# Kernel optimization log

Measured on AMD Instinct MI355X. Metric: run time of the kernel, lower is better.

Reference implementation:

```python
import jax, jax.numpy as jnp
import numpy as np

L, B, S, D, H, DK, F = 6, 4, 2048, 512, 8, 64, 2048


def setup_inputs() -> dict:
    key = jax.random.key(0)
    ks = iter(jax.random.split(key, 40))
    def rn(shape, scale=0.02):
        return jax.random.normal(next(ks), shape, jnp.float32) * scale
    inp = {
        "x": jax.random.normal(next(ks), (B, S, D), jnp.float32),
        "enc": jax.random.normal(next(ks), (B, S, D), jnp.float32),
    }
    for pre in ("sa", "ca"):
        inp[f"{pre}_wq"] = rn((L, D, H * DK)); inp[f"{pre}_bq"] = jnp.zeros((L, H * DK), jnp.float32)
        inp[f"{pre}_wk"] = rn((L, D, H * DK)); inp[f"{pre}_bk"] = jnp.zeros((L, H * DK), jnp.float32)
        inp[f"{pre}_wv"] = rn((L, D, H * DK)); inp[f"{pre}_bv"] = jnp.zeros((L, H * DK), jnp.float32)
        inp[f"{pre}_wo"] = rn((L, H * DK, D)); inp[f"{pre}_bo"] = jnp.zeros((L, D), jnp.float32)
    for i in (1, 2, 3):
        inp[f"ln{i}_g"] = jnp.ones((L, D), jnp.float32)
        inp[f"ln{i}_b"] = jnp.zeros((L, D), jnp.float32)
    inp["ff_w1"] = rn((L, D, F)); inp["ff_b1"] = jnp.zeros((L, F), jnp.float32)
    inp["ff_w2"] = rn((L, F, D)); inp["ff_b2"] = jnp.zeros((L, D), jnp.float32)
    return inp


def _layer_norm(z, g, b, eps=1e-5):
    m = z.mean(-1, keepdims=True)
    v = z.var(-1, keepdims=True)
    return (z - m) * jax.lax.rsqrt(v + eps) * g + b


def _mha(q_in, kv_in, wq, bq, wk, bk, wv, bv, wo, bo, causal_bias):
    b, s, _ = q_in.shape
    Q = (q_in @ wq + bq).reshape(b, s, H, DK)   # [B,S,H,DK]
    K = (kv_in @ wk + bk).reshape(b, s, H, DK)
    V = (kv_in @ wv + bv).reshape(b, s, H, DK)
    scores = jnp.einsum("bqhd,bkhd->bhqk", Q, K) / jnp.float32(DK) ** 0.5
    if causal_bias is not None:
        scores = scores + causal_bias  # additive -inf above diagonal
    w = jax.nn.softmax(scores, axis=-1)
    att = jnp.einsum("bhqk,bkhd->bqhd", w, V).reshape(b, s, H * DK)
    return att @ wo + bo


def reference(x, enc, sa_wq, sa_bq, sa_wk, sa_bk, sa_wv, sa_bv, sa_wo, sa_bo,
              ca_wq, ca_bq, ca_wk, ca_bk, ca_wv, ca_bv, ca_wo, ca_bo,
              ln1_g, ln1_b, ln2_g, ln2_b, ln3_g, ln3_b,
              ff_w1, ff_b1, ff_w2, ff_b2):
    s = x.shape[1]
    causal_bias = jnp.triu(jnp.full((s, s), -jnp.inf, jnp.float32), 1)

    params = (sa_wq, sa_bq, sa_wk, sa_bk, sa_wv, sa_bv, sa_wo, sa_bo,
              ca_wq, ca_bq, ca_wk, ca_bk, ca_wv, ca_bv, ca_wo, ca_bo,
              ln1_g, ln1_b, ln2_g, ln2_b, ln3_g, ln3_b,
              ff_w1, ff_b1, ff_w2, ff_b2)

    def block(h, p):
        (swq, sbq, swk, sbk, swv, sbv, swo, sbo,
         cwq, cbq, cwk, cbk, cwv, cbv, cwo, cbo,
         g1, b1, g2, b2, g3, b3, w1, bb1, w2, bb2) = p
        # masked self-attention + residual + LN  (faithful to source)
        x1 = _layer_norm(h + _mha(h, h, swq, sbq, swk, sbk, swv, sbv, swo, sbo, causal_bias), g1, b1)
        # cross-attention; residual comes from the BLOCK INPUT h (source bug kept)
        y = _layer_norm(h + _mha(x1, enc, cwq, cbq, cwk, cbk, cwv, cbv, cwo, cbo, None), g2, b2)
        # FFN; residual from x1 (source bug kept)
        out = _layer_norm(x1 + (jax.nn.relu(y @ w1 + bb1) @ w2 + bb2), g3, b3)
        return out, None

    out, _ = jax.lax.scan(block, x, params)
    return out
```

## Files before the change

kernel.cpp:

```cpp
#include <hip/hip_runtime.h>
#include <stdint.h>

#define LCOUNT 6
#define BB 4
#define SS 2048
#define DD 512
#define HH 8
#define DKK 64
#define FFDIM 2048
#define MM (BB*SS)

typedef __attribute__((ext_vector_type(8))) __bf16 bf16x8;
typedef __attribute__((ext_vector_type(4))) float f32x4;
typedef unsigned short u16;

__device__ __forceinline__ u16 f2bf(float f) {
  union { __bf16 h; u16 u; } v; v.h = (__bf16)f; return v.u;
}
__device__ __forceinline__ float bf2f(u16 u) {
  union { uint32_t u; float f; } v; v.u = ((uint32_t)u) << 16;
  return v.f;
}

__device__ __forceinline__ void gload_lds16(const u16* gsrc, u16* ldst) {
  __builtin_amdgcn_global_load_lds((const __attribute__((address_space(1))) char*)gsrc,
                                   (__attribute__((address_space(3))) char*)ldst, 16, 0, 0);
}

__global__ __launch_bounds__(256) void f2bf_kernel(const float* __restrict__ in,
                                                   u16* __restrict__ outp, int n) {
  int i = (blockIdx.x * 256 + threadIdx.x) * 8;
  if (i >= n) return;
  float4 a = *(const float4*)&in[i];
  float4 b = *(const float4*)&in[i + 4];
  union { u16 us[8]; uint4 v; } pk;
  pk.us[0] = f2bf(a.x); pk.us[1] = f2bf(a.y); pk.us[2] = f2bf(a.z); pk.us[3] = f2bf(a.w);
  pk.us[4] = f2bf(b.x); pk.us[5] = f2bf(b.y); pk.us[6] = f2bf(b.z); pk.us[7] = f2bf(b.w);
  *(uint4*)&outp[i] = pk.v;
}

__global__ __launch_bounds__(256) void bias_cat(const float* a, const float* b, const float* c,
                                                float* dst, int n, int total) {
  int i = blockIdx.x * 256 + threadIdx.x;
  if (i >= total) return;
  int parts = (c != nullptr) ? 3 : 2;
  int per = parts * n;
  int l = i / per, cc = i % per;
  const float* s = cc < n ? a : (cc < 2 * n ? b : c);
  dst[i] = s[l * n + (cc % n)];
}

__global__ __launch_bounds__(256) void wtrans(const float* __restrict__ W,
                                              u16* __restrict__ Wt, int K_, int N_,
                                              size_t lstride) {
  __shared__ float tile[64 * 65];
  const int l = blockIdx.z;
  const float* Wl = W + (size_t)l * K_ * N_;
  u16* Wtl = Wt + (size_t)l * lstride;
  const int n0 = blockIdx.x * 64, k0 = blockIdx.y * 64;
  const int tid = threadIdx.x;
  const int r = tid >> 2, c4 = (tid & 3) * 16;
#pragma unroll
  for (int j = 0; j < 16; j += 4) {
    float4 v = *(const float4*)&Wl[(size_t)(k0 + r) * N_ + n0 + c4 + j];
    tile[r * 65 + c4 + j + 0] = v.x;
    tile[r * 65 + c4 + j + 1] = v.y;
    tile[r * 65 + c4 + j + 2] = v.z;
    tile[r * 65 + c4 + j + 3] = v.w;
  }
  __syncthreads();
  const int nr = tid >> 2, kc = (tid & 3) * 16;
#pragma unroll
  for (int half = 0; half < 2; ++half) {
    union { u16 us[8]; uint4 v; } pk;
#pragma unroll
    for (int e = 0; e < 8; ++e) pk.us[e] = f2bf(tile[(kc + half * 8 + e) * 65 + nr]);
    *(uint4*)&Wtl[(size_t)(n0 + nr) * K_ + k0 + kc + half * 8] = pk.v;
  }
}

struct WtBatch {
  const float* src[8];
  u16* dst[8];
  unsigned long long lstr[8];
};
__global__ __launch_bounds__(256) void wtrans8(WtBatch wb) {
  __shared__ float tile[64 * 65];
  const int z = blockIdx.z;
  const int slot = z / 6, l = z - slot * 6;
  const float* Wl = wb.src[slot] + (size_t)l * 512 * 512;
  u16* Wtl = wb.dst[slot] + (size_t)l * wb.lstr[slot];
  const int n0 = blockIdx.x * 64, k0 = blockIdx.y * 64;
  const int tid = threadIdx.x;
  const int r = tid >> 2, c4 = (tid & 3) * 16;
#pragma unroll
  for (int j = 0; j < 16; j += 4) {
    float4 v = *(const float4*)&Wl[(size_t)(k0 + r) * 512 + n0 + c4 + j];
    tile[r * 65 + c4 + j + 0] = v.x;
    tile[r * 65 + c4 + j + 1] = v.y;
    tile[r * 65 + c4 + j + 2] = v.z;
    tile[r * 65 + c4 + j + 3] = v.w;
  }
  __syncthreads();
  const int nr = tid >> 2, kc = (tid & 3) * 16;
#pragma unroll
  for (int half = 0; half < 2; ++half) {
    union { u16 us[8]; uint4 v; } pk;
#pragma unroll
    for (int e = 0; e < 8; ++e) pk.us[e] = f2bf(tile[(kc + half * 8 + e) * 65 + nr]);
    *(uint4*)&Wtl[(size_t)(n0 + nr) * 512 + k0 + kc + half * 8] = pk.v;
  }
}

template <int BMT, int BNT, int BKT, bool RELU, bool VT>
__global__ __launch_bounds__(256)
void gemm_bt(const u16* __restrict__ A, const u16* __restrict__ Bt,
             const float* __restrict__ bias, u16* __restrict__ C,
             int N_, int K_, int CS, u16* __restrict__ vt, int vtc0,
             const u16* __restrict__ A2, int a2col) {
  constexpr int MR = BMT / 32;
  constexpr int NR = BNT / 32;
  constexpr int CH = BKT / 8;
  constexpr int RPR = 2048 / BKT;
  constexpr int KS = BKT / 32;
  __shared__ u16 As[BMT * BKT];
  __shared__ u16 Bs[BNT * BKT];
  const int tid = threadIdx.x;
  const int wid = tid >> 6, lane = tid & 63;
  const int l15 = lane & 15, g = lane >> 4;
  const int wr = wid >> 1, wc = wid & 1;
  const int lrow = (CH == 8) ? (lane >> 3) : (lane >> 4);
  const int lch  = lane & (CH - 1);
  const int wrows = 64 / CH;
  const int lin = blockIdx.x + gridDim.x * blockIdx.y;
  const int nwg = gridDim.x * gridDim.y;
  const int swz = (lin & 7) * (nwg >> 3) + (lin >> 3);
  const int brow = (swz / gridDim.x) * BMT;
  const int bcol = (swz % gridDim.x) * BNT;
  const u16* Ap = (A2 != nullptr && bcol >= a2col) ? A2 : A;

  f32x4 acc[MR][NR];
#pragma unroll
  for (int m = 0; m < MR; ++m)
#pragma unroll
    for (int n = 0; n < NR; ++n) acc[m][n] = (f32x4){0.f, 0.f, 0.f, 0.f};

  for (int kt = 0; kt < K_; kt += BKT) {
#pragma unroll
    for (int r = 0; r < BMT / RPR; ++r) {
      int row = r * RPR + wid * wrows + lrow;
      int slot = lch ^ (row & 7);
      gload_lds16(Ap + (size_t)(brow + row) * K_ + kt + slot * 8,
                  &As[r * 2048 + wid * 512]);
    }
#pragma unroll
    for (int r = 0; r < BNT / RPR; ++r) {
      int row = r * RPR + wid * wrows + lrow;
      int slot = lch ^ (row & 7);
      gload_lds16(Bt + (size_t)(bcol + row) * K_ + kt + slot * 8,
                  &Bs[r * 2048 + wid * 512]);
    }
    __syncthreads();
#pragma unroll
    for (int ks = 0; ks < KS; ++ks) {
      bf16x8 af[MR], bfr[NR];
#pragma unroll
      for (int m = 0; m < MR; ++m) {
        int row = wr * (BMT / 2) + m * 16 + l15;
        int slot = (ks * 4 + g) ^ (row & 7);
        af[m] = *(const bf16x8*)&As[row * BKT + slot * 8];
      }
#pragma unroll
      for (int n = 0; n < NR; ++n) {
        int row = wc * (BNT / 2) + n * 16 + l15;
        int slot = (ks * 4 + g) ^ (row & 7);
        bfr[n] = *(const bf16x8*)&Bs[row * BKT + slot * 8];
      }
#pragma unroll
      for (int m = 0; m < MR; ++m)
#pragma unroll
        for (int n = 0; n < NR; ++n)
          acc[m][n] = __builtin_amdgcn_mfma_f32_16x16x32_bf16(af[m], bfr[n], acc[m][n], 0, 0, 0);
    }
    __syncthreads();
  }
#pragma unroll
  for (int n = 0; n < NR; ++n) {
    int col = bcol + wc * (BNT / 2) + n * 16 + l15;
    float bv = bias ? bias[col] : 0.f;
    if (VT && col >= vtc0) {
      int hh = (col - vtc0) >> 6, dd = (col - vtc0) & 63;
#pragma unroll
      for (int m = 0; m < MR; ++m) {
        int s0g = brow + wr * (BMT / 2) + m * 16 + g * 4;
        int bb = s0g >> 11, ss = s0g & (SS - 1);
        union { u16 us[4]; uint2 v; } pk;
#pragma unroll
        for (int r = 0; r < 4; ++r) pk.us[r] = f2bf(acc[m][n][r] + bv);
        *(uint2*)&vt[(((size_t)(bb * HH + hh)) * DKK + dd) * SS + ss] = pk.v;
      }
    } else {
#pragma unroll
      for (int m = 0; m < MR; ++m) {
#pragma unroll
        for (int r = 0; r < 4; ++r) {
          int rowg = brow + wr * (BMT / 2) + m * 16 + g * 4 + r;
          float v = acc[m][n][r] + bv;
          if (RELU) v = fmaxf(v, 0.f);
          C[(size_t)rowg * CS + col] = f2bf(v);
        }
      }
    }
  }
}

__global__ __launch_bounds__(256)
void gemm_ln(const u16* __restrict__ A, const u16* __restrict__ Bt,
             const float* __restrict__ bias, const u16* __restrict__ Res,
             const float* __restrict__ gamma, const float* __restrict__ beta,
             u16* __restrict__ Out, float* __restrict__ Ofp, int K_) {
  __shared__ u16 As[16 * 64];
  __shared__ u16 Bs[512 * 64];
  __shared__ float red[4][16][2];
  const int tid = threadIdx.x;
  const int wid = tid >> 6, lane = tid & 63;
  const int l15 = lane & 15, g = lane >> 4;
  const int lin = blockIdx.x;
  const int swz = (lin & 7) * (gridDim.x >> 3) + (lin >> 3);
  const int brow = swz * 16;
  const int lrow8 = lane >> 3, lch = lane & 7;

  f32x4 acc[8];
#pragma unroll
  for (int n = 0; n < 8; ++n) acc[n] = (f32x4){0.f, 0.f, 0.f, 0.f};

  for (int kt = 0; kt < K_; kt += 64) {
#pragma unroll
    for (int r = 0; r < 17; ++r) {
      int u = wid + 4 * r;
      if (u < 66) {
        if (u < 2) {
          int row = u * 8 + lrow8;
          int slot = lch ^ (row & 7);
          gload_lds16(A + (size_t)(brow + row) * K_ + kt + slot * 8, &As[u * 512]);
        } else {
          int row = (u - 2) * 8 + lrow8;
          int slot = lch ^ (row & 7);
          gload_lds16(Bt + (size_t)row * K_ + kt + slot * 8, &Bs[(u - 2) * 512]);
        }
      }
    }
    __syncthreads();
#pragma unroll
    for (int ks = 0; ks < 2; ++ks) {
      bf16x8 af = *(const bf16x8*)&As[l15 * 64 + (((ks * 4 + g) ^ (l15 & 7)) * 8)];
#pragma unroll
      for (int n = 0; n < 8; ++n) {
        int c = wid * 128 + n * 16 + l15;
        bf16x8 bfr = *(const bf16x8*)&Bs[c * 64 + (((ks * 4 + g) ^ (c & 7)) * 8)];
        acc[n] = __builtin_amdgcn_mfma_f32_16x16x32_bf16(af, bfr, acc[n], 0, 0, 0);
      }
    }
    __syncthreads();
  }
#pragma unroll
  for (int rd = 0; rd < 4; ++rd) {
    int off = rd * 2048 + tid * 8;
    int row = off >> 9, col = off & 511;
    uint4 v = *(const uint4*)&Res[(size_t)(brow + row) * DD + col];
    *(uint4*)&Bs[row * 520 + col] = v;
  }
  __syncthreads();
  float z[8][4];
  float s[4] = {0.f, 0.f, 0.f, 0.f}, s2[4] = {0.f, 0.f, 0.f, 0.f};
#pragma unroll
  for (int n = 0; n < 8; ++n) {
    int col = wid * 128 + n * 16 + l15;
    float bv = bias[col];
#pragma unroll
    for (int r = 0; r < 4; ++r) {
      int rl = g * 4 + r;
      float x = acc[n][r] + bv + bf2f(Bs[rl * 520 + col]);
      z[n][r] = x; s[r] += x; s2[r] += x * x;
    }
  }
#pragma unroll
  for (int r = 0; r < 4; ++r) {
    s[r] += __shfl_xor(s[r], 1);  s2[r] += __shfl_xor(s2[r], 1);
    s[r] += __shfl_xor(s[r], 2);  s2[r] += __shfl_xor(s2[r], 2);
    s[r] += __shfl_xor(s[r], 4);  s2[r] += __shfl_xor(s2[r], 4);
    s[r] += __shfl_xor(s[r], 8);  s2[r] += __shfl_xor(s2[r], 8);
  }
  if (l15 == 0) {
#pragma unroll
    for (int r = 0; r < 4; ++r) {
      red[wid][g * 4 + r][0] = s[r];
      red[wid][g * 4 + r][1] = s2[r];
    }
  }
  __syncthreads();
  float mean[4], rs[4];
#pragma unroll
  for (int r = 0; r < 4; ++r) {
    int rl = g * 4 + r;
    float ts  = red[0][rl][0] + red[1][rl][0] + red[2][rl][0] + red[3][rl][0];
    float ts2 = red[0][rl][1] + red[1][rl][1] + red[2][rl][1] + red[3][rl][1];
    float mn = ts * (1.f / 512.f);
    float var = ts2 * (1.f / 512.f) - mn * mn;
    mean[r] = mn; rs[r] = rsqrtf(var + 1e-5f);
  }
#pragma unroll
  for (int n = 0; n < 8; ++n) {
    int col = wid * 128 + n * 16 + l15;
    float gm = gamma[col], bt = beta[col];
#pragma unroll
    for (int r = 0; r < 4; ++r) {
      int rowg = brow + g * 4 + r;
      float o = (z[n][r] - mean[r]) * rs[r] * gm + bt;
      Out[(size_t)rowg * DD + col] = f2bf(o);
      if (Ofp) Ofp[(size_t)rowg * DD + col] = o;
    }
  }
}

template <bool CAUSAL>
__global__ __launch_bounds__(256, 4)
void attn_kernel(const u16* __restrict__ Qm, const u16* __restrict__ Km,
                 const u16* __restrict__ Vt, u16* __restrict__ Om, int qks) {
  __shared__ u16 Ks[2][64 * 64];
  __shared__ u16 Vs[2][64 * 64];
  __shared__ u16 Ps[4][16 * 64];
  const int lin = blockIdx.x;
  const int bh = (lin & 7) * 4 + ((lin >> 3) >> 5);
  const int qc = (lin >> 3) & 31;
  const int qb = (qc & 1) ? (31 - (qc >> 1)) : (qc >> 1);
  const int h = bh & 7, b = bh >> 3;
  const int tid = threadIdx.x, wid = tid >> 6, lane = tid & 63;
  const int l15 = lane & 15, g = lane >> 4;
  const int qstart = qb * 64;
  const size_t qbase = ((size_t)b * SS) * qks + h * DKK;
  const size_t vtbase = (size_t)(b * HH + h) * DKK * SS;
  const size_t obase = ((size_t)b * SS) * DD + h * DKK;
  u16* psw = &Ps[wid][0];
  const int srow = wid * 8 + (lane >> 3);
  const int sslot = lane & 7;
  const int qg = qstart + wid * 16 + l15;
  const int pswz = (l15 & 7) << 1;
  const float SC = 0.18033688f;

  const u16* kp = Km + qbase;
  const u16* vp = Vt + vtbase;

  bf16x8 qf[2];
#pragma unroll
  for (int ks = 0; ks < 2; ++ks)
    qf[ks] = *(const bf16x8*)&Qm[qbase + (size_t)qg * qks + ks * 32 + g * 8];

  f32x4 oacc[4];
#pragma unroll
  for (int nb = 0; nb < 4; ++nb) oacc[nb] = (f32x4){0.f, 0.f, 0.f, 0.f};
  float m_run = -3.0e38f, l_run = 0.f;

  const int T = CAUSAL ? (qb + 1) : (SS / 64);

#pragma unroll
  for (int r = 0; r < 2; ++r) {
    int row = r * 32 + srow;
    int slot = sslot ^ (row & 7);
    gload_lds16(kp + (size_t)row * qks + slot * 8, &Ks[0][r * 2048 + wid * 512]);
    gload_lds16(vp + (size_t)row * SS + slot * 8, &Vs[0][r * 2048 + wid * 512]);
  }
  __syncthreads();

  int cur = 0;
  for (int t = 0; t < T; ++t) {
    const int kstart = t * 64;
    if (t + 1 < T) {
#pragma unroll
      for (int r = 0; r < 2; ++r) {
        int row = r * 32 + srow;
        int slot = sslot ^ (row & 7);
        gload_lds16(kp + (size_t)(kstart + 64 + row) * qks + slot * 8,
                    &Ks[cur ^ 1][r * 2048 + wid * 512]);
        gload_lds16(vp + (size_t)row * SS + kstart + 64 + slot * 8,
                    &Vs[cur ^ 1][r * 2048 + wid * 512]);
      }
    }
    f32x4 sacc[4];
#pragma unroll
    for (int nb = 0; nb < 4; ++nb) sacc[nb] = (f32x4){0.f, 0.f, 0.f, 0.f};
    __builtin_amdgcn_s_setprio(1);
#pragma unroll
    for (int nb = 0; nb < 4; ++nb) {
      int row = nb * 16 + l15;
#pragma unroll
      for (int ks = 0; ks < 2; ++ks) {
        bf16x8 kf = *(const bf16x8*)&Ks[cur][row * 64 + (((ks * 4 + g) ^ (row & 7)) * 8)];
        sacc[nb] = __builtin_amdgcn_mfma_f32_16x16x32_bf16(kf, qf[ks], sacc[nb], 0, 0, 0);
      }
    }
    __builtin_amdgcn_s_setprio(0);
    if (CAUSAL && t == T - 1) {
#pragma unroll
      for (int nb = 0; nb < 4; ++nb)
#pragma unroll
        for (int r = 0; r < 4; ++r)
          if ((kstart + nb * 16 + g * 4 + r) > qg) sacc[nb][r] = -3.0e38f;
    }
    f32x4 m4 = sacc[0];
#pragma unroll
    for (int nb = 1; nb < 4; ++nb) {
      m4[0] = fmaxf(m4[0], sacc[nb][0]); m4[1] = fmaxf(m4[1], sacc[nb][1]);
      m4[2] = fmaxf(m4[2], sacc[nb][2]); m4[3] = fmaxf(m4[3], sacc[nb][3]);
    }
    float mx = fmaxf(fmaxf(m4[0], m4[1]), fmaxf(m4[2], m4[3]));
    mx = fmaxf(mx, __shfl_xor(mx, 16));
    mx = fmaxf(mx, __shfl_xor(mx, 32));
    const bool skip = __all(mx <= m_run + 64.0f);
    float mnew = skip ? m_run : fmaxf(m_run, mx);
    float mc = mnew * SC;
    float s = 0.f;
#pragma unroll
    for (int nb = 0; nb < 4; ++nb) {
#pragma unroll
      for (int r = 0; r < 4; ++r) {
        float e = __builtin_amdgcn_exp2f(sacc[nb][r] * SC - mc);
        sacc[nb][r] = e; s += e;
      }
    }
    s += __shfl_xor(s, 16);
    s += __shfl_xor(s, 32);
    if (skip) {
      l_run += s;
    } else {
      float resc = __builtin_amdgcn_exp2f((m_run - mnew) * SC);
      l_run = l_run * resc + s;
      m_run = mnew;
      float ro[4];
#pragma unroll
      for (int r = 0; r < 4; ++r) ro[r] = __shfl(resc, g * 4 + r);
#pragma unroll
      for (int nb = 0; nb < 4; ++nb)
#pragma unroll
        for (int r = 0; r < 4; ++r) oacc[nb][r] *= ro[r];
    }
#pragma unroll
    for (int nb = 0; nb < 4; ++nb) {
      union { u16 us[4]; uint2 v; } pk;
#pragma unroll
      for (int r = 0; r < 4; ++r) pk.us[r] = f2bf(sacc[nb][r]);
      int cp = (nb * 4 + g) ^ pswz;
      *(uint2*)&psw[l15 * 64 + cp * 4] = pk.v;
    }
    bf16x8 pf[2];
#pragma unroll
    for (int ks = 0; ks < 2; ++ks) {
      int cp0 = (8 * ks + 2 * g) ^ pswz;
      pf[ks] = *(const bf16x8*)&psw[l15 * 64 + cp0 * 4];
    }
    __builtin_amdgcn_s_setprio(1);
#pragma unroll
    for (int nb = 0; nb < 4; ++nb) {
      int row = nb * 16 + l15;
#pragma unroll
      for (int ks = 0; ks < 2; ++ks) {
        bf16x8 vf = *(const bf16x8*)&Vs[cur][row * 64 + (((ks * 4 + g) ^ (row & 7)) * 8)];
        oacc[nb] = __builtin_amdgcn_mfma_f32_16x16x32_bf16(pf[ks], vf, oacc[nb], 0, 0, 0);
      }
    }
    __builtin_amdgcn_s_setprio(0);
    __syncthreads();
    cur ^= 1;
  }
  float linv = 1.f / l_run;
  float io[4];
#pragma unroll
  for (int r = 0; r < 4; ++r) io[r] = __shfl(linv, g * 4 + r);
#pragma unroll
  for (int nb = 0; nb < 4; ++nb) {
#pragma unroll
    for (int r = 0; r < 4; ++r) {
      Om[obase + (size_t)(qstart + wid * 16 + g * 4 + r) * DD + nb * 16 + l15] =
          f2bf(oacc[nb][r] * io[r]);
    }
  }
}

extern "C" void kernel_launch(void* const* d_in, const int* in_sizes, int n_in,
                              void* d_out, int out_size, void* d_ws, size_t ws_size,
                              hipStream_t stream) {
  const float* x   = (const float*)d_in[0];
  const float* enc = (const float*)d_in[1];
  const float* sa_w[4] = {(const float*)d_in[2], (const float*)d_in[4], (const float*)d_in[6], (const float*)d_in[8]};
  const float* sa_b[4] = {(const float*)d_in[3], (const float*)d_in[5], (const float*)d_in[7], (const float*)d_in[9]};
  const float* ca_w[4] = {(const float*)d_in[10], (const float*)d_in[12], (const float*)d_in[14], (const float*)d_in[16]};
  const float* ca_b[4] = {(const float*)d_in[11], (const float*)d_in[13], (const float*)d_in[15], (const float*)d_in[17]};
  const float* ln_g[3] = {(const float*)d_in[18], (const float*)d_in[20], (const float*)d_in[22]};
  const float* ln_b[3] = {(const float*)d_in[19], (const float*)d_in[21], (const float*)d_in[23]};
  const float* ffw1 = (const float*)d_in[24];
  const float* ffb1 = (const float*)d_in[25];
  const float* ffw2 = (const float*)d_in[26];
  const float* ffb2 = (const float*)d_in[27];

  char* ws = (char*)d_ws;
  size_t o = 0;
  auto take = [&](size_t bytes) {
    void* p = ws + o;
    o += (bytes + 255) & ~(size_t)255;
    return p;
  };
  u16* wqkv  = (u16*)take((size_t)LCOUNT * 1536 * 512 * 2);
  u16* wca   = (u16*)take((size_t)LCOUNT * 1536 * 512 * 2);
  u16* wosa  = (u16*)take((size_t)LCOUNT * 512 * 512 * 2);
  u16* woca  = (u16*)take((size_t)LCOUNT * 512 * 512 * 2);
  u16* w1t   = (u16*)take((size_t)LCOUNT * 512 * 2048 * 2);
  u16* w2t   = (u16*)take((size_t)LCOUNT * 2048 * 512 * 2);
  float* bqkv = (float*)take((size_t)LCOUNT * 1536 * 4);
  float* bca  = (float*)take((size_t)LCOUNT * 1536 * 4);
  u16* Hb   = (u16*)take((size_t)MM * 512 * 2);
  u16* Eb   = (u16*)take((size_t)MM * 512 * 2);
  u16* QKVb = (u16*)take((size_t)MM * 1536 * 2);
  u16* Ab   = (u16*)take((size_t)MM * 512 * 2);
  u16* X1b  = (u16*)take((size_t)MM * 512 * 2);
  u16* Yb   = (u16*)take((size_t)MM * 512 * 2);
  u16* Fb   = (u16*)take((size_t)MM * 2048 * 2);
  u16* Vtb  = Fb;

  f2bf_kernel<<<2048, 256, 0, stream>>>(x, Hb, MM * 512);
  f2bf_kernel<<<2048, 256, 0, stream>>>(enc, Eb, MM * 512);
  WtBatch wb;
  wb.src[0] = sa_w[0]; wb.dst[0] = wqkv;              wb.lstr[0] = (size_t)1536 * 512;
  wb.src[1] = sa_w[1]; wb.dst[1] = wqkv + 512 * 512;  wb.lstr[1] = (size_t)1536 * 512;
  wb.src[2] = sa_w[2]; wb.dst[2] = wqkv + 1024 * 512; wb.lstr[2] = (size_t)1536 * 512;
  wb.src[3] = sa_w[3]; wb.dst[3] = wosa;              wb.lstr[3] = (size_t)512 * 512;
  wb.src[4] = ca_w[0]; wb.dst[4] = wca;               wb.lstr[4] = (size_t)1536 * 512;
  wb.src[5] = ca_w[1]; wb.dst[5] = wca + 512 * 512;   wb.lstr[5] = (size_t)1536 * 512;
  wb.src[6] = ca_w[2]; wb.dst[6] = wca + 1024 * 512;  wb.lstr[6] = (size_t)1536 * 512;
  wb.src[7] = ca_w[3]; wb.dst[7] = woca;              wb.lstr[7] = (size_t)512 * 512;
  wtrans8<<<dim3(8, 8, 48), 256, 0, stream>>>(wb);
  wtrans<<<dim3(32, 8, LCOUNT), 256, 0, stream>>>(ffw1, w1t, 512, 2048, (size_t)2048 * 512);
  wtrans<<<dim3(8, 32, LCOUNT), 256, 0, stream>>>(ffw2, w2t, 2048, 512, (size_t)512 * 2048);
  bias_cat<<<36, 256, 0, stream>>>(sa_b[0], sa_b[1], sa_b[2], bqkv, 512, LCOUNT * 1536);
  bias_cat<<<36, 256, 0, stream>>>(ca_b[0], ca_b[1], ca_b[2], bca, 512, LCOUNT * 1536);

  for (int l = 0; l < LCOUNT; ++l) {
    const size_t w512 = (size_t)l * 512 * 512;
    const size_t wff = (size_t)l * 512 * 2048;
    gemm_bt<128, 128, 64, false, true><<<dim3(12, 64), 256, 0, stream>>>(
        Hb, wqkv + (size_t)l * 1536 * 512, bqkv + l * 1536, QKVb, 1536, 512, 1536, Vtb, 1024,
        nullptr, 0);
    attn_kernel<true><<<dim3(1024), 256, 0, stream>>>(QKVb, QKVb + 512, Vtb, Ab, 1536);
    gemm_ln<<<dim3(512), 256, 0, stream>>>(Ab, wosa + w512, sa_b[3] + l * 512, Hb,
                                           ln_g[0] + l * 512, ln_b[0] + l * 512,
                                           X1b, nullptr, 512);
    gemm_bt<128, 128, 64, false, true><<<dim3(12, 64), 256, 0, stream>>>(
        X1b, wca + (size_t)l * 1536 * 512, bca + l * 1536, QKVb, 1536, 512, 1536, Vtb, 1024,
        Eb, 512);
    attn_kernel<false><<<dim3(1024), 256, 0, stream>>>(QKVb, QKVb + 512, Vtb, Ab, 1536);
    gemm_ln<<<dim3(512), 256, 0, stream>>>(Ab, woca + w512, ca_b[3] + l * 512, Hb,
                                           ln_g[1] + l * 512, ln_b[1] + l * 512,
                                           Yb, nullptr, 512);
    gemm_bt<128, 128, 64, true, false><<<dim3(16, 64), 256, 0, stream>>>(
        Yb, w1t + wff, ffb1 + l * 2048, Fb, 2048, 512, 2048, nullptr, 0, nullptr, 0);
    gemm_ln<<<dim3(512), 256, 0, stream>>>(Fb, w2t + wff, ffb2 + l * 512, X1b,
                                           ln_g[2] + l * 512, ln_b[2] + l * 512,
                                           Hb, (l == LCOUNT - 1) ? (float*)d_out : nullptr,
                                           2048);
  }
}
```

Baseline: 1.750 ms.

## Split FFN2 GEMM+LayerNorm into tiled GEMM plus separate LN kernel; merge setup kernels

The fused FFN-down GEMM+LayerNorm (K=2048) is replaced by a plain gemm_bt with a 64x128x128 tile and a 512-block grid, writing a bf16 intermediate. A new row-wise LayerNorm kernel then adds the residual and normalizes. This trades the fused kernel's low parallelism (512 blocks covering full 512-wide rows) for more blocks, at the cost of an extra write and read of the intermediate and a bf16 rounding of the pre-LN sum. Setup conversions, FFN weight transposes and bias concatenations are also merged into fewer launches.

Measured after the change: 1.723 ms. Within noise of the previous version (-1.5%).

```diff
diff --git a/kernel.cpp b/kernel.cpp
--- a/kernel.cpp
+++ b/kernel.cpp
@@ -27,56 +27,34 @@
                                    (__attribute__((address_space(3))) char*)ldst, 16, 0, 0);
 }
 
-__global__ __launch_bounds__(256) void f2bf_kernel(const float* __restrict__ in,
-                                                   u16* __restrict__ outp, int n) {
+__global__ __launch_bounds__(256) void f2bf2(const float* __restrict__ x,
+                                             const float* __restrict__ enc,
+                                             u16* __restrict__ Hb, u16* __restrict__ Eb) {
   int i = (blockIdx.x * 256 + threadIdx.x) * 8;
-  if (i >= n) return;
-  float4 a = *(const float4*)&in[i];
-  float4 b = *(const float4*)&in[i + 4];
+  const int half = MM * 512;
+  const float* src = (i < half) ? x : enc;
+  u16* dst = (i < half) ? Hb : Eb;
+  int j = (i < half) ? i : i - half;
+  float4 a = *(const float4*)&src[j];
+  float4 b = *(const float4*)&src[j + 4];
   union { u16 us[8]; uint4 v; } pk;
   pk.us[0] = f2bf(a.x); pk.us[1] = f2bf(a.y); pk.us[2] = f2bf(a.z); pk.us[3] = f2bf(a.w);
   pk.us[4] = f2bf(b.x); pk.us[5] = f2bf(b.y); pk.us[6] = f2bf(b.z); pk.us[7] = f2bf(b.w);
-  *(uint4*)&outp[i] = pk.v;
-}
-
-__global__ __launch_bounds__(256) void bias_cat(const float* a, const float* b, const float* c,
-                                                float* dst, int n, int total) {
+  *(uint4*)&dst[j] = pk.v;
+}
+
+__global__ __launch_bounds__(256)
+void bias_cat2(const float* a0, const float* a1, const float* a2,
+               const float* c0, const float* c1, const float* c2,
+               float* dqkv, float* dca) {
   int i = blockIdx.x * 256 + threadIdx.x;
-  if (i >= total) return;
-  int parts = (c != nullptr) ? 3 : 2;
-  int per = parts * n;
-  int l = i / per, cc = i % per;
-  const float* s = cc < n ? a : (cc < 2 * n ? b : c);
-  dst[i] = s[l * n + (cc % n)];
-}
-
-__global__ __launch_bounds__(256) void wtrans(const float* __restrict__ W,
-                                              u16* __restrict__ Wt, int K_, int N_,
-                                              size_t lstride) {
-  __shared__ float tile[64 * 65];
-  const int l = blockIdx.z;
-  const float* Wl = W + (size_t)l * K_ * N_;
-  u16* Wtl = Wt + (size_t)l * lstride;
-  const int n0 = blockIdx.x * 64, k0 = blockIdx.y * 64;
-  const int tid = threadIdx.x;
-  const int r = tid >> 2, c4 = (tid & 3) * 16;
-#pragma unroll
-  for (int j = 0; j < 16; j += 4) {
-    float4 v = *(const float4*)&Wl[(size_t)(k0 + r) * N_ + n0 + c4 + j];
-    tile[r * 65 + c4 + j + 0] = v.x;
-    tile[r * 65 + c4 + j + 1] = v.y;
-    tile[r * 65 + c4 + j + 2] = v.z;
-    tile[r * 65 + c4 + j + 3] = v.w;
-  }
-  __syncthreads();
-  const int nr = tid >> 2, kc = (tid & 3) * 16;
-#pragma unroll
-  for (int half = 0; half < 2; ++half) {
-    union { u16 us[8]; uint4 v; } pk;
-#pragma unroll
-    for (int e = 0; e < 8; ++e) pk.us[e] = f2bf(tile[(kc + half * 8 + e) * 65 + nr]);
-    *(uint4*)&Wtl[(size_t)(n0 + nr) * K_ + k0 + kc + half * 8] = pk.v;
-  }
+  const int half = LCOUNT * 1536;
+  if (i >= 2 * half) return;
+  bool ca = i >= half;
+  int j = ca ? i - half : i;
+  int l = j / 1536, cc = j % 1536;
+  const float* s = cc < 512 ? (ca ? c0 : a0) : cc < 1024 ? (ca ? c1 : a1) : (ca ? c2 : a2);
+  (ca ? dca : dqkv)[j] = s[l * 512 + (cc & 511)];
 }
 
 struct WtBatch {
@@ -109,6 +87,40 @@
 #pragma unroll
     for (int e = 0; e < 8; ++e) pk.us[e] = f2bf(tile[(kc + half * 8 + e) * 65 + nr]);
     *(uint4*)&Wtl[(size_t)(n0 + nr) * 512 + k0 + kc + half * 8] = pk.v;
+  }
+}
+
+__global__ __launch_bounds__(256)
+void wtrans_ffn(const float* __restrict__ w1, const float* __restrict__ w2,
+                u16* __restrict__ w1t, u16* __restrict__ w2t) {
+  __shared__ float tile[64 * 65];
+  const int z = blockIdx.y;
+  const bool is2 = z >= 6;
+  const int l = is2 ? z - 6 : z;
+  const float* Wl = (is2 ? w2 : w1) + (size_t)l * 512 * 2048;
+  u16* Wtl = (is2 ? w2t : w1t) + (size_t)l * 512 * 2048;
+  const int K_ = is2 ? 2048 : 512, N_ = is2 ? 512 : 2048;
+  const int bx = blockIdx.x;
+  const int n0 = is2 ? (bx & 7) * 64 : (bx & 31) * 64;
+  const int k0 = is2 ? (bx >> 3) * 64 : (bx >> 5) * 64;
+  const int tid = threadIdx.x;
+  const int r = tid >> 2, c4 = (tid & 3) * 16;
+#pragma unroll
+  for (int j = 0; j < 16; j += 4) {
+    float4 v = *(const float4*)&Wl[(size_t)(k0 + r) * N_ + n0 + c4 + j];
+    tile[r * 65 + c4 + j + 0] = v.x;
+    tile[r * 65 + c4 + j + 1] = v.y;
+    tile[r * 65 + c4 + j + 2] = v.z;
+    tile[r * 65 + c4 + j + 3] = v.w;
+  }
+  __syncthreads();
+  const int nr = tid >> 2, kc = (tid & 3) * 16;
+#pragma unroll
+  for (int half = 0; half < 2; ++half) {
+    union { u16 us[8]; uint4 v; } pk;
+#pragma unroll
+    for (int e = 0; e < 8; ++e) pk.us[e] = f2bf(tile[(kc + half * 8 + e) * 65 + nr]);
+    *(uint4*)&Wtl[(size_t)(n0 + nr) * K_ + k0 + kc + half * 8] = pk.v;
   }
 }
 
@@ -323,6 +335,40 @@
   }
 }
 
+__global__ __launch_bounds__(256)
+void ln_kernel(const u16* __restrict__ A, const u16* __restrict__ Bv,
+               const float* __restrict__ gamma, const float* __restrict__ beta,
+               u16* __restrict__ out_bf, float* __restrict__ out_f32) {
+  const int row = blockIdx.x * 4 + (threadIdx.x >> 6);
+  const int lane = threadIdx.x & 63;
+  uint4 av = *(const uint4*)&A[(size_t)row * DD + lane * 8];
+  uint4 bv = *(const uint4*)&Bv[(size_t)row * DD + lane * 8];
+  const u16* au = (const u16*)&av;
+  const u16* bu = (const u16*)&bv;
+  float z[8], s = 0.f, s2 = 0.f;
+#pragma unroll
+  for (int j = 0; j < 8; ++j) {
+    float x = bf2f(au[j]) + bf2f(bu[j]);
+    z[j] = x; s += x; s2 += x * x;
+  }
+#pragma unroll
+  for (int off = 1; off < 64; off <<= 1) {
+    s += __shfl_xor(s, off);
+    s2 += __shfl_xor(s2, off);
+  }
+  float mean = s * (1.f / 512.f);
+  float var = s2 * (1.f / 512.f) - mean * mean;
+  float rs = rsqrtf(var + 1e-5f);
+  union { u16 us[8]; uint4 v; } pk;
+#pragma unroll
+  for (int j = 0; j < 8; ++j) {
+    float o = (z[j] - mean) * rs * gamma[lane * 8 + j] + beta[lane * 8 + j];
+    pk.us[j] = f2bf(o);
+    if (out_f32) out_f32[(size_t)row * DD + lane * 8 + j] = o;
+  }
+  *(uint4*)&out_bf[(size_t)row * DD + lane * 8] = pk.v;
+}
+
 template <bool CAUSAL>
 __global__ __launch_bounds__(256, 4)
 void attn_kernel(const u16* __restrict__ Qm, const u16* __restrict__ Km,
@@ -521,13 +567,13 @@
   u16* Eb   = (u16*)take((size_t)MM * 512 * 2);
   u16* QKVb = (u16*)take((size_t)MM * 1536 * 2);
   u16* Ab   = (u16*)take((size_t)MM * 512 * 2);
+  u16* Pb   = (u16*)take((size_t)MM * 512 * 2);
   u16* X1b  = (u16*)take((size_t)MM * 512 * 2);
   u16* Yb   = (u16*)take((size_t)MM * 512 * 2);
   u16* Fb   = (u16*)take((size_t)MM * 2048 * 2);
   u16* Vtb  = Fb;
 
-  f2bf_kernel<<<2048, 256, 0, stream>>>(x, Hb, MM * 512);
-  f2bf_kernel<<<2048, 256, 0, stream>>>(enc, Eb, MM * 512);
+  f2bf2<<<4096, 256, 0, stream>>>(x, enc, Hb, Eb);
   WtBatch wb;
   wb.src[0] = sa_w[0]; wb.dst[0] = wqkv;              wb.lstr[0] = (size_t)1536 * 512;
   wb.src[1] = sa_w[1]; wb.dst[1] = wqkv + 512 * 512;  wb.lstr[1] = (size_t)1536 * 512;
@@ -538,10 +584,9 @@
   wb.src[6] = ca_w[2]; wb.dst[6] = wca + 1024 * 512;  wb.lstr[6] = (size_t)1536 * 512;
   wb.src[7] = ca_w[3]; wb.dst[7] = woca;              wb.lstr[7] = (size_t)512 * 512;
   wtrans8<<<dim3(8, 8, 48), 256, 0, stream>>>(wb);
-  wtrans<<<dim3(32, 8, LCOUNT), 256, 0, stream>>>(ffw1, w1t, 512, 2048, (size_t)2048 * 512);
-  wtrans<<<dim3(8, 32, LCOUNT), 256, 0, stream>>>(ffw2, w2t, 2048, 512, (size_t)512 * 2048);
-  bias_cat<<<36, 256, 0, stream>>>(sa_b[0], sa_b[1], sa_b[2], bqkv, 512, LCOUNT * 1536);
-  bias_cat<<<36, 256, 0, stream>>>(ca_b[0], ca_b[1], ca_b[2], bca, 512, LCOUNT * 1536);
+  wtrans_ffn<<<dim3(256, 12), 256, 0, stream>>>(ffw1, ffw2, w1t, w2t);
+  bias_cat2<<<72, 256, 0, stream>>>(sa_b[0], sa_b[1], sa_b[2], ca_b[0], ca_b[1], ca_b[2],
+                                    bqkv, bca);
 
   for (int l = 0; l < LCOUNT; ++l) {
     const size_t w512 = (size_t)l * 512 * 512;
@@ -562,9 +607,9 @@
                                            Yb, nullptr, 512);
     gemm_bt<128, 128, 64, true, false><<<dim3(16, 64), 256, 0, stream>>>(
         Yb, w1t + wff, ffb1 + l * 2048, Fb, 2048, 512, 2048, nullptr, 0, nullptr, 0);
-    gemm_ln<<<dim3(512), 256, 0, stream>>>(Fb, w2t + wff, ffb2 + l * 512, X1b,
-                                           ln_g[2] + l * 512, ln_b[2] + l * 512,
-                                           Hb, (l == LCOUNT - 1) ? (float*)d_out : nullptr,
-                                           2048);
-  }
-}
+    gemm_bt<64, 128, 128, false, false><<<dim3(4, 128), 256, 0, stream>>>(
+        Fb, w2t + wff, ffb2 + l * 512, Pb, 512, 2048, 512, nullptr, 0, nullptr, 0);
+    ln_kernel<<<MM / 4, 256, 0, stream>>>(X1b, Pb, ln_g[2] + l * 512, ln_b[2] + l * 512, Hb,
+                                          (l == LCOUNT - 1) ? (float*)d_out : nullptr);
+  }
+}
```
